# Optimization experiments

Hardware: AMD Instinct MI355X
Metric: run time of the kernel (lower is better)

## Reference

```python
import jax, jax.numpy as jnp
import numpy as np

NUM_ITERS = 3
NUM_SLOTS = 8
D = 128
MLP_HIDDEN = 128
EPS = 1e-8
LN_EPS = 1e-5
B, N = 64, 4096


def _layer_norm(x, g, b):
    m = jnp.mean(x, axis=-1, keepdims=True)
    v = jnp.mean(jnp.square(x - m), axis=-1, keepdims=True)
    return (x - m) * jax.lax.rsqrt(v + LN_EPS) * g + b


def setup_inputs() -> dict:
    key = jax.random.key(0)
    ks = jax.random.split(key, 16)
    s = 1.0 / np.sqrt(D)
    inp = {
        "x": jax.random.normal(ks[0], (B, N, D), jnp.float32),
        "slots_init": jax.random.normal(ks[1], (B, NUM_SLOTS, D), jnp.float32),
        "Wq": jax.random.normal(ks[2], (D, D), jnp.float32) * s,
        "bq": jnp.zeros((D,), jnp.float32),
        "Wk": jax.random.normal(ks[3], (D, D), jnp.float32) * s,
        "bk": jnp.zeros((D,), jnp.float32),
        "Wv": jax.random.normal(ks[4], (D, D), jnp.float32) * s,
        "bv": jnp.zeros((D,), jnp.float32),
        "g_in": jnp.ones((D,), jnp.float32), "b_in": jnp.zeros((D,), jnp.float32),
        "g_slot": jnp.ones((D,), jnp.float32), "b_slot": jnp.zeros((D,), jnp.float32),
        "g_mlp": jnp.ones((D,), jnp.float32), "b_mlp": jnp.zeros((D,), jnp.float32),
        "W1": jax.random.normal(ks[5], (MLP_HIDDEN, D), jnp.float32) * s,
        "b1": jnp.zeros((MLP_HIDDEN,), jnp.float32),
        "W2": jax.random.normal(ks[6], (D, MLP_HIDDEN), jnp.float32) * (1.0 / np.sqrt(MLP_HIDDEN)),
        "b2": jnp.zeros((D,), jnp.float32),
        "W_ih": jax.random.normal(ks[7], (3 * D, D), jnp.float32) * s,
        "W_hh": jax.random.normal(ks[8], (3 * D, D), jnp.float32) * s,
        "b_ih": jnp.zeros((3 * D,), jnp.float32),
        "b_hh": jnp.zeros((3 * D,), jnp.float32),
    }
    return inp


def _gru_cell(x, h, W_ih, W_hh, b_ih, b_hh):
    # torch.nn.GRUCell semantics
    gi = x @ W_ih.T + b_ih          # [.., 3D]
    gh = h @ W_hh.T + b_hh
    i_r, i_z, i_n = jnp.split(gi, 3, axis=-1)
    h_r, h_z, h_n = jnp.split(gh, 3, axis=-1)
    r = jax.nn.sigmoid(i_r + h_r)
    z = jax.nn.sigmoid(i_z + h_z)
    n = jnp.tanh(i_n + r * h_n)
    return (1.0 - z) * n + z * h


def reference(x, slots_init, Wq, bq, Wk, bk, Wv, bv, g_in, b_in, g_slot, b_slot,
              g_mlp, b_mlp, W1, b1, W2, b2, W_ih, W_hh, b_ih, b_hh):
    xn = _layer_norm(x, g_in, b_in)                 # [B,N,D]
    keys = xn @ Wk.T + bk                            # [B,N,D]
    values = xn @ Wv.T + bv                          # [B,N,D]
    scale = D ** -0.5
    slots = slots_init                               # [B,K,D]
    for _ in range(NUM_ITERS):
        prev = slots
        s = _layer_norm(slots, g_slot, b_slot)
        q = s @ Wq.T + bq                            # [B,K,D]
        logits = jnp.einsum('bid,bkd->bik', q, keys) * scale  # [B,K,N]
        attn = jax.nn.softmax(logits, axis=1)        # softmax over SLOT axis
        attn = attn + EPS
        attn = attn / jnp.sum(attn, axis=-1, keepdims=True)
        updates = jnp.einsum('bkd,bik->bid', values, attn)     # [B,K,D]
        slots = _gru_cell(updates.reshape(-1, D), prev.reshape(-1, D),
                          W_ih, W_hh, b_ih, b_hh).reshape(x.shape[0], -1, D)
        h = jax.nn.relu(_layer_norm(slots, g_mlp, b_mlp) @ W1.T + b1)
        slots = slots + (h @ W2.T + b2)
    return slots
```

## Files before the change

### kernel.cpp

```cpp
#include <hip/hip_runtime.h>
#include <hip/hip_bf16.h>

#define B_ 64
#define N_ 4096
#define KS 8
#define NCH 16
#define TP 136
#define LNEPS 1e-5f
#define EPSA 1e-8f
#define SCALE 0.08838834764831845f

typedef short short8  __attribute__((ext_vector_type(8)));
typedef short short4v __attribute__((ext_vector_type(4)));
typedef float f32x4   __attribute__((ext_vector_type(4)));

__device__ __forceinline__ unsigned short f2bf(float f) {
  union { float f; unsigned u; } v; v.f = f;
  unsigned r = v.u + 0x7fffu + ((v.u >> 16) & 1u);
  return (unsigned short)(r >> 16);
}
__device__ __forceinline__ float bflo(unsigned u) {
  union { unsigned u; float f; } c; c.u = u << 16; return c.f;
}
__device__ __forceinline__ float bfhi(unsigned u) {
  union { unsigned u; float f; } c; c.u = u & 0xffff0000u; return c.f;
}
__device__ __forceinline__ float sigmf(float x) { return 1.f / (1.f + __expf(-x)); }

__global__ __launch_bounds__(256) void prep_big(
    const float* __restrict__ Wih, const float* __restrict__ Whh,
    const float* __restrict__ Wq,  const float* __restrict__ Wk,
    const float* __restrict__ Wv,  const float* __restrict__ W1,
    const float* __restrict__ W2,
    const float* __restrict__ g_slot, const float* __restrict__ g_mlp,
    float* __restrict__ WgT, float* __restrict__ Mq,
    float* __restrict__ W1gT, float* __restrict__ W2T)
{
  int id = blockIdx.x * 256 + threadIdx.x;
  if (id < 49152) {
    int j = id >> 7, d = id & 127;
    float a = 0.f;
    for (int k = 0; k < 128; k++) a += Wih[j*128 + k] * Wv[k*128 + d];
    WgT[d*768 + j] = a;
  } else if (id < 65536) {
    int k = id - 49152; int d = k >> 7, t = k & 127;
    float a = 0.f;
    for (int j = 0; j < 128; j++) a += Wk[j*128 + t] * Wq[j*128 + d];
    Mq[d*128 + t] = a * SCALE * g_slot[d];
  } else if (id < 114688) {
    int k = id - 65536; int j = k >> 7, d = k & 127;
    WgT[d*768 + 384 + j] = Whh[j*128 + d];
  } else if (id < 131072) {
    int k = id - 114688; int t = k >> 7, d = k & 127;
    W1gT[d*128 + t] = W1[t*128 + d] * g_mlp[d];
  } else if (id < 147456) {
    int k = id - 131072; int t = k >> 7, d = k & 127;
    W2T[d*128 + t] = W2[t*128 + d];
  }
}

__global__ __launch_bounds__(256) void prep_small(
    const float* __restrict__ Wq, const float* __restrict__ Wk,
    const float* __restrict__ Wih, const float* __restrict__ W1,
    const float* __restrict__ bq, const float* __restrict__ bk,
    const float* __restrict__ bv, const float* __restrict__ b_ih,
    const float* __restrict__ b_hh, const float* __restrict__ b1,
    const float* __restrict__ b_mlp, const float* __restrict__ b_slot,
    const float* __restrict__ g_slot,
    float* __restrict__ cq_vec, float* __restrict__ wqcg,
    float* __restrict__ qc0g, float* __restrict__ bg, float* __restrict__ b1f)
{
  __shared__ float u[128], wqcr[128];
  int t = threadIdx.x;
  if (t < 128) {
    float a = bq[t];
    for (int d = 0; d < 128; d++) a += Wq[t*128 + d] * b_slot[d];
    u[t] = a;
  } else {
    int d = t - 128;
    float a = 0.f;
    for (int j = 0; j < 128; j++) a += Wq[j*128 + d] * bk[j];
    wqcr[d] = a * SCALE;
  }
  __syncthreads();
  if (t < 128) {
    float a = 0.f;
    for (int j = 0; j < 128; j++) a += Wk[j*128 + t] * u[j];
    cq_vec[t] = a * SCALE;
    wqcg[t] = wqcr[t] * g_slot[t];
  } else {
    int d = t - 128;
    float a = b1[d];
    for (int k = 0; k < 128; k++) a += W1[d*128 + k] * b_mlp[k];
    b1f[d] = a;
  }
  if (t < 64) {
    float v = wqcr[t]*b_slot[t] + wqcr[t+64]*b_slot[t+64]
            + SCALE*(bq[t]*bk[t] + bq[t+64]*bk[t+64]);
    #pragma unroll
    for (int st = 1; st < 64; st <<= 1) v += __shfl_xor(v, st);
    if (t == 0) *qc0g = v;
  }
  #pragma unroll
  for (int p = 0; p < 3; p++) {
    int j = t + p*256;
    if (j < 384) {
      float a = b_ih[j];
      for (int k = 0; k < 128; k++) a += Wih[j*128 + k] * bv[k];
      bg[j] = a;
    } else if (j < 768) {
      bg[j] = b_hh[j - 384];
    }
  }
}

__global__ __launch_bounds__(256) void ln_kernel(
    const float* __restrict__ x, const float* __restrict__ g_in, const float* __restrict__ b_in,
    unsigned short* __restrict__ xn)
{
  int tid = threadIdx.x;
  int rw = tid >> 2, cp = tid & 3;
  size_t row = (size_t)blockIdx.x * 64 + rw;
  const float* xrow = x + row * 128;
  float4 v[8];
  float s = 0.f, s2 = 0.f;
  #pragma unroll
  for (int i = 0; i < 8; i++) {
    v[i] = *(const float4*)(xrow + (cp + 4*i)*4);
    s  += v[i].x + v[i].y + v[i].z + v[i].w;
    s2 += v[i].x*v[i].x + v[i].y*v[i].y + v[i].z*v[i].z + v[i].w*v[i].w;
  }
  s += __shfl_xor(s, 1); s2 += __shfl_xor(s2, 1);
  s += __shfl_xor(s, 2); s2 += __shfl_xor(s2, 2);
  float mean = s * (1.f/128.f);
  float rstd = rsqrtf(s2 * (1.f/128.f) - mean*mean + LNEPS);
  #pragma unroll
  for (int i = 0; i < 8; i++) {
    int col = (cp + 4*i)*4;
    float4 gg = *(const float4*)(g_in + col);
    float4 bb = *(const float4*)(b_in + col);
    short4v pk;
    pk[0] = (short)f2bf((v[i].x - mean)*rstd*gg.x + bb.x);
    pk[1] = (short)f2bf((v[i].y - mean)*rstd*gg.y + bb.y);
    pk[2] = (short)f2bf((v[i].z - mean)*rstd*gg.z + bb.z);
    pk[3] = (short)f2bf((v[i].w - mean)*rstd*gg.w + bb.w);
    *(short4v*)(xn + row*128 + col) = pk;
  }
}

__global__ __launch_bounds__(64) void q_init_kernel(
    const float* __restrict__ slots_in, const float* __restrict__ Mq,
    const float* __restrict__ cq_vec, const float* __restrict__ wqcg,
    const float* __restrict__ qc0g,
    float* __restrict__ qt, float* __restrict__ qc)
{
  __shared__ float lnr[128];
  int row = blockIdx.x, t = threadIdx.x;
  float a = slots_in[row*128 + t], b = slots_in[row*128 + 64 + t];
  float s = a + b, s2 = a*a + b*b;
  #pragma unroll
  for (int st = 1; st < 64; st <<= 1) { s += __shfl_xor(s, st); s2 += __shfl_xor(s2, st); }
  float mean = s * (1.f/128.f);
  float rstd = rsqrtf(s2 * (1.f/128.f) - mean*mean + LNEPS);
  lnr[t] = (a - mean)*rstd; lnr[t+64] = (b - mean)*rstd;
  __syncthreads();
  float a0 = cq_vec[t], a1 = cq_vec[t+64];
  for (int d = 0; d < 128; d++) {
    float l = lnr[d];
    a0 += Mq[d*128 + t] * l;
    a1 += Mq[d*128 + 64 + t] * l;
  }
  qt[row*128 + t] = a0; qt[row*128 + 64 + t] = a1;
  float vq = wqcg[t]*lnr[t] + wqcg[t+64]*lnr[t+64];
  #pragma unroll
  for (int st = 1; st < 64; st <<= 1) vq += __shfl_xor(vq, st);
  if (t == 0) qc[row] = vq + *qc0g;
}

__global__ __launch_bounds__(256) void attn_kernel(
    const unsigned short* __restrict__ xn,
    const float* __restrict__ qt, const float* __restrict__ qc,
    float* __restrict__ Upart, float* __restrict__ Spart)
{
  __shared__ union ShMem {
    unsigned short xt[4][16][TP];
    float ured[4][8][128];
  } sh;
  __shared__ __align__(16) float pb[4][16][8];
  __shared__ float sred[4][8];

  const int tid = threadIdx.x;
  const int w = tid >> 6, lane = tid & 63;
  const int chunk = blockIdx.x, batch = blockIdx.y;
  const int m = lane & 15, quad = lane >> 4;

  short8 afrag[4];
  if (m < KS) {
    const float* qp = qt + (batch*KS + m)*128 + quad*8;
    #pragma unroll
    for (int kc = 0; kc < 4; kc++) {
      short8 a;
      #pragma unroll
      for (int j = 0; j < 8; j++) a[j] = (short)f2bf(qp[kc*32 + j]);
      afrag[kc] = a;
    }
  } else {
    #pragma unroll
    for (int kc = 0; kc < 4; kc++) {
      short8 a;
      #pragma unroll
      for (int j = 0; j < 8; j++) a[j] = 0;
      afrag[kc] = a;
    }
  }
  float creg[4];
  #pragma unroll
  for (int r = 0; r < 4; r++) creg[r] = qc[batch*KS + ((quad*4 + r) & 7)];

  float u0[8], u1[8], sac[4];
  #pragma unroll
  for (int i = 0; i < 8; i++) { u0[i] = 0.f; u1[i] = 0.f; }
  #pragma unroll
  for (int r = 0; r < 4; r++) sac[r] = 0.f;

  const unsigned short* xbase =
      xn + ((size_t)batch*N_ + chunk*256 + w*64 + m)*128 + quad*8;

  short8 cur[4], nxt[4];
  #pragma unroll
  for (int kc = 0; kc < 4; kc++) cur[kc] = *(const short8*)(xbase + kc*32);

  for (int g = 0; g < 4; g++) {
    if (g < 3) {
      #pragma unroll
      for (int kc = 0; kc < 4; kc++)
        nxt[kc] = *(const short8*)(xbase + (g+1)*2048 + kc*32);
    }
    #pragma unroll
    for (int kc = 0; kc < 4; kc++)
      *(short8*)&sh.xt[w][m][kc*32 + quad*8] = cur[kc];

    f32x4 acc = {0.f, 0.f, 0.f, 0.f};
    #pragma unroll
    for (int kc = 0; kc < 4; kc++)
      acc = __builtin_amdgcn_mfma_f32_16x16x32_bf16(afrag[kc], cur[kc], acc, 0, 0, 0);

    float l[4], o[4];
    #pragma unroll
    for (int r = 0; r < 4; r++) l[r] = acc[r] + creg[r];
    #pragma unroll
    for (int r = 0; r < 4; r++) o[r] = __shfl_xor(l[r], 16);
    float mx = fmaxf(fmaxf(fmaxf(l[0], l[1]), fmaxf(l[2], l[3])),
                     fmaxf(fmaxf(o[0], o[1]), fmaxf(o[2], o[3])));
    float e0 = __expf(l[0]-mx), e1 = __expf(l[1]-mx), e2 = __expf(l[2]-mx), e3 = __expf(l[3]-mx);
    float den = e0+e1+e2+e3 + __expf(o[0]-mx)+__expf(o[1]-mx)+__expf(o[2]-mx)+__expf(o[3]-mx);
    float rd = 1.f / den;
    float p0 = e0*rd + EPSA, p1 = e1*rd + EPSA, p2 = e2*rd + EPSA, p3 = e3*rd + EPSA;
    sac[0] += p0; sac[1] += p1; sac[2] += p2; sac[3] += p3;
    if (lane < 32) {
      float4 pv; pv.x = p0; pv.y = p1; pv.z = p2; pv.w = p3;
      *(float4*)&pb[w][m][quad*4] = pv;
    }

    #pragma unroll
    for (int t = 0; t < 16; t++) {
      float4 pA = *(const float4*)&pb[w][t][0];
      float4 pB = *(const float4*)&pb[w][t][4];
      unsigned vp = *(const unsigned*)&sh.xt[w][t][lane*2];
      float f0 = bflo(vp), f1 = bfhi(vp);
      u0[0] += pA.x*f0; u1[0] += pA.x*f1;
      u0[1] += pA.y*f0; u1[1] += pA.y*f1;
      u0[2] += pA.z*f0; u1[2] += pA.z*f1;
      u0[3] += pA.w*f0; u1[3] += pA.w*f1;
      u0[4] += pB.x*f0; u1[4] += pB.x*f1;
      u0[5] += pB.y*f0; u1[5] += pB.y*f1;
      u0[6] += pB.z*f0; u1[6] += pB.z*f1;
      u0[7] += pB.w*f0; u1[7] += pB.w*f1;
    }
    #pragma unroll
    for (int kc = 0; kc < 4; kc++) cur[kc] = nxt[kc];
  }

  #pragma unroll
  for (int st = 1; st < 16; st <<= 1) {
    #pragma unroll
    for (int r = 0; r < 4; r++) sac[r] += __shfl_xor(sac[r], st);
  }
  if (lane == 0)  { sred[w][0]=sac[0]; sred[w][1]=sac[1]; sred[w][2]=sac[2]; sred[w][3]=sac[3]; }
  if (lane == 16) { sred[w][4]=sac[0]; sred[w][5]=sac[1]; sred[w][6]=sac[2]; sred[w][7]=sac[3]; }

  __syncthreads();
  #pragma unroll
  for (int i = 0; i < 8; i++)
    *(float2*)&sh.ured[w][i][lane*2] = make_float2(u0[i], u1[i]);
  __syncthreads();

  {
    const float* ur = &sh.ured[0][0][0];
    int i4 = tid * 4;
    float4 a = *(const float4*)(ur + i4);
    float4 b = *(const float4*)(ur + 1024 + i4);
    float4 c = *(const float4*)(ur + 2048 + i4);
    float4 d = *(const float4*)(ur + 3072 + i4);
    float4 o4;
    o4.x = a.x+b.x+c.x+d.x; o4.y = a.y+b.y+c.y+d.y;
    o4.z = a.z+b.z+c.z+d.z; o4.w = a.w+b.w+c.w+d.w;
    *(float4*)(Upart + (size_t)(batch*NCH + chunk)*1024 + i4) = o4;
    if (tid < 8)
      Spart[(batch*NCH + chunk)*8 + tid] =
        sred[0][tid] + sred[1][tid] + sred[2][tid] + sred[3][tid];
  }
}

__global__ __launch_bounds__(256) void update_kernel(
    const float* __restrict__ slots_in, float* __restrict__ slots_out,
    const float* __restrict__ Upart, const float* __restrict__ Spart,
    const float* __restrict__ WgT, const float* __restrict__ bg,
    const float* __restrict__ W1gT, const float* __restrict__ b1f,
    const float* __restrict__ W2T, const float* __restrict__ b2,
    const float* __restrict__ Mq, const float* __restrict__ cq_vec,
    const float* __restrict__ wqcg, const float* __restrict__ qc0g,
    float* __restrict__ qt, float* __restrict__ qc)
{
  __shared__ float bu[128], hb[128], gg[768];
  __shared__ float s1[128], lnr[128], hmv[128], s2v[128], lnr2[128];
  __shared__ float stats[2], sSum;
  int row = blockIdx.x, t = threadIdx.x;
  int batch = row >> 3, slot = row & 7;

  float usum = 0.f;
  if (t < 128) {
    const float* Up = Upart + ((size_t)(batch*NCH)*8 + slot)*128 + t;
    #pragma unroll
    for (int c = 0; c < NCH; c++) usum += Up[(size_t)c*1024];
  } else {
    hb[t-128] = slots_in[row*128 + (t-128)];
    if (t < 192) {
      int l2 = t - 128;
      float sv = (l2 < NCH) ? Spart[(batch*NCH + l2)*8 + slot] : 0.f;
      #pragma unroll
      for (int st = 1; st < 16; st <<= 1) sv += __shfl_xor(sv, st);
      if (l2 == 0) sSum = sv;
    }
  }
  __syncthreads();
  if (t < 128) bu[t] = usum / sSum;
  __syncthreads();
  {
    float a0 = bg[t], a1 = bg[t+256], a2 = bg[t+512];
    const float* v1p = (t < 128) ? bu : hb;
    for (int d = 0; d < 128; d++) {
      float sd = bu[d], hd = hb[d], vd = v1p[d];
      const float* wr = WgT + d*768 + t;
      a0 += sd * wr[0];
      a1 += vd * wr[256];
      a2 += hd * wr[512];
    }
    gg[t] = a0; gg[t+256] = a1; gg[t+512] = a2;
  }
  __syncthreads();
  if (t < 128) {
    float r = sigmf(gg[t] + gg[384+t]);
    float z = sigmf(gg[128+t] + gg[512+t]);
    float n = tanhf(gg[256+t] + r * gg[640+t]);
    s1[t] = (1.f - z)*n + z*hb[t];
  }
  __syncthreads();
  if (t < 64) {
    float a = s1[t], b = s1[t+64];
    float s = a + b, s2 = a*a + b*b;
    #pragma unroll
    for (int st = 1; st < 64; st <<= 1) { s += __shfl_xor(s, st); s2 += __shfl_xor(s2, st); }
    if (t == 0) { float mean = s*(1.f/128.f); stats[0] = mean;
                  stats[1] = rsqrtf(s2*(1.f/128.f) - mean*mean + LNEPS); }
  }
  __syncthreads();
  if (t < 128) lnr[t] = (s1[t] - stats[0])*stats[1];
  __syncthreads();
  if (t < 128) {
    float a = b1f[t];
    for (int d = 0; d < 128; d++) a += W1gT[d*128 + t]*lnr[d];
    hmv[t] = fmaxf(a, 0.f);
  }
  __syncthreads();
  if (t < 128) {
    float a = s1[t] + b2[t];
    for (int d = 0; d < 128; d++) a += W2T[d*128 + t]*hmv[d];
    s2v[t] = a;
    slots_out[row*128 + t] = a;
  }
  __syncthreads();
  if (t < 64) {
    float a = s2v[t], b = s2v[t+64];
    float s = a + b, s2 = a*a + b*b;
    #pragma unroll
    for (int st = 1; st < 64; st <<= 1) { s += __shfl_xor(s, st); s2 += __shfl_xor(s2, st); }
    if (t == 0) { float mean = s*(1.f/128.f); stats[0] = mean;
                  stats[1] = rsqrtf(s2*(1.f/128.f) - mean*mean + LNEPS); }
  }
  __syncthreads();
  if (t < 128) lnr2[t] = (s2v[t] - stats[0])*stats[1];
  __syncthreads();
  if (t < 128) {
    float a = cq_vec[t];
    for (int d = 0; d < 128; d++) a += Mq[d*128 + t]*lnr2[d];
    qt[row*128 + t] = a;
  }
  if (t < 64) {
    float v = wqcg[t]*lnr2[t] + wqcg[t+64]*lnr2[t+64];
    #pragma unroll
    for (int st = 1; st < 64; st <<= 1) v += __shfl_xor(v, st);
    if (t == 0) qc[row] = v + *qc0g;
  }
}

extern "C" void kernel_launch(void* const* d_in, const int* in_sizes, int n_in,
                              void* d_out, int out_size, void* d_ws, size_t ws_size,
                              hipStream_t stream) {
  const float* x          = (const float*)d_in[0];
  const float* slots_init = (const float*)d_in[1];
  const float* Wq   = (const float*)d_in[2];
  const float* bq   = (const float*)d_in[3];
  const float* Wk   = (const float*)d_in[4];
  const float* bk   = (const float*)d_in[5];
  const float* Wv   = (const float*)d_in[6];
  const float* bv   = (const float*)d_in[7];
  const float* g_in = (const float*)d_in[8];
  const float* b_in = (const float*)d_in[9];
  const float* g_slot = (const float*)d_in[10];
  const float* b_slot = (const float*)d_in[11];
  const float* g_mlp  = (const float*)d_in[12];
  const float* b_mlp  = (const float*)d_in[13];
  const float* W1   = (const float*)d_in[14];
  const float* b1   = (const float*)d_in[15];
  const float* W2   = (const float*)d_in[16];
  const float* b2   = (const float*)d_in[17];
  const float* Wih  = (const float*)d_in[18];
  const float* Whh  = (const float*)d_in[19];
  const float* b_ih = (const float*)d_in[20];
  const float* b_hh = (const float*)d_in[21];

  char* p = (char*)d_ws;
  unsigned short* xn = (unsigned short*)p; p += (size_t)B_*N_*128*2;
  float* qt    = (float*)p; p += (size_t)B_*KS*128*4;
  float* qc    = (float*)p; p += (size_t)B_*KS*4 + 1024;
  float* slots = (float*)p; p += (size_t)B_*KS*128*4;
  float* Upart = (float*)p; p += (size_t)B_*NCH*KS*128*4;
  float* Spart = (float*)p; p += (size_t)B_*NCH*KS*4 + 1024;
  float* WgT   = (float*)p; p += 98304*4;
  float* Mq    = (float*)p; p += 16384*4;
  float* W1gT  = (float*)p; p += 16384*4;
  float* W2T   = (float*)p; p += 16384*4;
  float* cq_vec= (float*)p; p += 128*4;
  float* wqcg  = (float*)p; p += 128*4;
  float* qc0g  = (float*)p; p += 256;
  float* bg    = (float*)p; p += 768*4;
  float* b1f   = (float*)p; p += 128*4;

  ln_kernel<<<4096, 256, 0, stream>>>(x, g_in, b_in, xn);
  prep_big<<<576, 256, 0, stream>>>(Wih, Whh, Wq, Wk, Wv, W1, W2, g_slot, g_mlp,
                                    WgT, Mq, W1gT, W2T);
  prep_small<<<1, 256, 0, stream>>>(Wq, Wk, Wih, W1, bq, bk, bv, b_ih, b_hh, b1,
                                    b_mlp, b_slot, g_slot, cq_vec, wqcg, qc0g, bg, b1f);
  q_init_kernel<<<512, 64, 0, stream>>>(slots_init, Mq, cq_vec, wqcg, qc0g, qt, qc);

  attn_kernel<<<dim3(NCH, B_), 256, 0, stream>>>(xn, qt, qc, Upart, Spart);
  update_kernel<<<512, 256, 0, stream>>>(slots_init, slots, Upart, Spart,
      WgT, bg, W1gT, b1f, W2T, b2, Mq, cq_vec, wqcg, qc0g, qt, qc);

  attn_kernel<<<dim3(NCH, B_), 256, 0, stream>>>(xn, qt, qc, Upart, Spart);
  update_kernel<<<512, 256, 0, stream>>>(slots, slots, Upart, Spart,
      WgT, bg, W1gT, b1f, W2T, b2, Mq, cq_vec, wqcg, qc0g, qt, qc);

  attn_kernel<<<dim3(NCH, B_), 256, 0, stream>>>(xn, qt, qc, Upart, Spart);
  update_kernel<<<512, 256, 0, stream>>>(slots, (float*)d_out, Upart, Spart,
      WgT, bg, W1gT, b1f, W2T, b2, Mq, cq_vec, wqcg, qc0g, qt, qc);

  (void)in_sizes; (void)n_in; (void)out_size; (void)ws_size;
}
```

Before: 395.1 us.

## Fuse input layernorm into first attention pass and halve attention chunk count

Input layernorm now runs inside the first attention kernel: it reads fp32 x, normalizes each row into shared memory as bf16, writes xn back for later iterations, and consumes it directly. This removes the separate LN kernel and the first re-read of xn. Attention chunks drop from 16 to 8 per batch, so each block handles 512 tokens with double-buffered prefetch two groups ahead. The two prep kernels are merged into one launch. The trade-off is fewer blocks (512), which lowers parallelism, and the fused first pass carries heavier per-block work.

Result: slower. 1.240 ms (+213.8%).

```diff
diff --git a/kernel.cpp b/kernel.cpp
--- a/kernel.cpp
+++ b/kernel.cpp
@@ -4,7 +4,7 @@
 #define B_ 64
 #define N_ 4096
 #define KS 8
-#define NCH 16
+#define ACH 8
 #define TP 136
 #define LNEPS 1e-5f
 #define EPSA 1e-8f
@@ -27,15 +27,66 @@
 }
 __device__ __forceinline__ float sigmf(float x) { return 1.f / (1.f + __expf(-x)); }
 
-__global__ __launch_bounds__(256) void prep_big(
+__global__ __launch_bounds__(256) void prep_kernel(
     const float* __restrict__ Wih, const float* __restrict__ Whh,
     const float* __restrict__ Wq,  const float* __restrict__ Wk,
     const float* __restrict__ Wv,  const float* __restrict__ W1,
     const float* __restrict__ W2,
     const float* __restrict__ g_slot, const float* __restrict__ g_mlp,
+    const float* __restrict__ bq, const float* __restrict__ bk,
+    const float* __restrict__ bv, const float* __restrict__ b_ih,
+    const float* __restrict__ b_hh, const float* __restrict__ b1,
+    const float* __restrict__ b_mlp, const float* __restrict__ b_slot,
     float* __restrict__ WgT, float* __restrict__ Mq,
-    float* __restrict__ W1gT, float* __restrict__ W2T)
-{
+    float* __restrict__ W1gT, float* __restrict__ W2T,
+    float* __restrict__ cq_vec, float* __restrict__ wqcg,
+    float* __restrict__ qc0g, float* __restrict__ bg, float* __restrict__ b1f)
+{
+  if (blockIdx.x == 576) {
+    __shared__ float u[128], wqcr[128];
+    int t = threadIdx.x;
+    if (t < 128) {
+      float a = bq[t];
+      for (int d = 0; d < 128; d++) a += Wq[t*128 + d] * b_slot[d];
+      u[t] = a;
+    } else {
+      int d = t - 128;
+      float a = 0.f;
+      for (int j = 0; j < 128; j++) a += Wq[j*128 + d] * bk[j];
+      wqcr[d] = a * SCALE;
+    }
+    __syncthreads();
+    if (t < 128) {
+      float a = 0.f;
+      for (int j = 0; j < 128; j++) a += Wk[j*128 + t] * u[j];
+      cq_vec[t] = a * SCALE;
+      wqcg[t] = wqcr[t] * g_slot[t];
+    } else {
+      int d = t - 128;
+      float a = b1[d];
+      for (int k = 0; k < 128; k++) a += W1[d*128 + k] * b_mlp[k];
+      b1f[d] = a;
+    }
+    if (t < 64) {
+      float v = wqcr[t]*b_slot[t] + wqcr[t+64]*b_slot[t+64]
+              + SCALE*(bq[t]*bk[t] + bq[t+64]*bk[t+64]);
+      #pragma unroll
+      for (int st = 1; st < 64; st <<= 1) v += __shfl_xor(v, st);
+      if (t == 0) *qc0g = v;
+    }
+    #pragma unroll
+    for (int p = 0; p < 3; p++) {
+      int j = t + p*256;
+      if (j < 384) {
+        float a = b_ih[j];
+        for (int k = 0; k < 128; k++) a += Wih[j*128 + k] * bv[k];
+        bg[j] = a;
+      } else if (j < 768) {
+        bg[j] = b_hh[j - 384];
+      }
+    }
+    return;
+  }
   int id = blockIdx.x * 256 + threadIdx.x;
   if (id < 49152) {
     int j = id >> 7, d = id & 127;
@@ -59,95 +110,6 @@
   }
 }
 
-__global__ __launch_bounds__(256) void prep_small(
-    const float* __restrict__ Wq, const float* __restrict__ Wk,
-    const float* __restrict__ Wih, const float* __restrict__ W1,
-    const float* __restrict__ bq, const float* __restrict__ bk,
-    const float* __restrict__ bv, const float* __restrict__ b_ih,
-    const float* __restrict__ b_hh, const float* __restrict__ b1,
-    const float* __restrict__ b_mlp, const float* __restrict__ b_slot,
-    const float* __restrict__ g_slot,
-    float* __restrict__ cq_vec, float* __restrict__ wqcg,
-    float* __restrict__ qc0g, float* __restrict__ bg, float* __restrict__ b1f)
-{
-  __shared__ float u[128], wqcr[128];
-  int t = threadIdx.x;
-  if (t < 128) {
-    float a = bq[t];
-    for (int d = 0; d < 128; d++) a += Wq[t*128 + d] * b_slot[d];
-    u[t] = a;
-  } else {
-    int d = t - 128;
-    float a = 0.f;
-    for (int j = 0; j < 128; j++) a += Wq[j*128 + d] * bk[j];
-    wqcr[d] = a * SCALE;
-  }
-  __syncthreads();
-  if (t < 128) {
-    float a = 0.f;
-    for (int j = 0; j < 128; j++) a += Wk[j*128 + t] * u[j];
-    cq_vec[t] = a * SCALE;
-    wqcg[t] = wqcr[t] * g_slot[t];
-  } else {
-    int d = t - 128;
-    float a = b1[d];
-    for (int k = 0; k < 128; k++) a += W1[d*128 + k] * b_mlp[k];
-    b1f[d] = a;
-  }
-  if (t < 64) {
-    float v = wqcr[t]*b_slot[t] + wqcr[t+64]*b_slot[t+64]
-            + SCALE*(bq[t]*bk[t] + bq[t+64]*bk[t+64]);
-    #pragma unroll
-    for (int st = 1; st < 64; st <<= 1) v += __shfl_xor(v, st);
-    if (t == 0) *qc0g = v;
-  }
-  #pragma unroll
-  for (int p = 0; p < 3; p++) {
-    int j = t + p*256;
-    if (j < 384) {
-      float a = b_ih[j];
-      for (int k = 0; k < 128; k++) a += Wih[j*128 + k] * bv[k];
-      bg[j] = a;
-    } else if (j < 768) {
-      bg[j] = b_hh[j - 384];
-    }
-  }
-}
-
-__global__ __launch_bounds__(256) void ln_kernel(
-    const float* __restrict__ x, const float* __restrict__ g_in, const float* __restrict__ b_in,
-    unsigned short* __restrict__ xn)
-{
-  int tid = threadIdx.x;
-  int rw = tid >> 2, cp = tid & 3;
-  size_t row = (size_t)blockIdx.x * 64 + rw;
-  const float* xrow = x + row * 128;
-  float4 v[8];
-  float s = 0.f, s2 = 0.f;
-  #pragma unroll
-  for (int i = 0; i < 8; i++) {
-    v[i] = *(const float4*)(xrow + (cp + 4*i)*4);
-    s  += v[i].x + v[i].y + v[i].z + v[i].w;
-    s2 += v[i].x*v[i].x + v[i].y*v[i].y + v[i].z*v[i].z + v[i].w*v[i].w;
-  }
-  s += __shfl_xor(s, 1); s2 += __shfl_xor(s2, 1);
-  s += __shfl_xor(s, 2); s2 += __shfl_xor(s2, 2);
-  float mean = s * (1.f/128.f);
-  float rstd = rsqrtf(s2 * (1.f/128.f) - mean*mean + LNEPS);
-  #pragma unroll
-  for (int i = 0; i < 8; i++) {
-    int col = (cp + 4*i)*4;
-    float4 gg = *(const float4*)(g_in + col);
-    float4 bb = *(const float4*)(b_in + col);
-    short4v pk;
-    pk[0] = (short)f2bf((v[i].x - mean)*rstd*gg.x + bb.x);
-    pk[1] = (short)f2bf((v[i].y - mean)*rstd*gg.y + bb.y);
-    pk[2] = (short)f2bf((v[i].z - mean)*rstd*gg.z + bb.z);
-    pk[3] = (short)f2bf((v[i].w - mean)*rstd*gg.w + bb.w);
-    *(short4v*)(xn + row*128 + col) = pk;
-  }
-}
-
 __global__ __launch_bounds__(64) void q_init_kernel(
     const float* __restrict__ slots_in, const float* __restrict__ Mq,
     const float* __restrict__ cq_vec, const float* __restrict__ wqcg,
@@ -177,24 +139,87 @@
   if (t == 0) qc[row] = vq + *qc0g;
 }
 
-__global__ __launch_bounds__(256) void attn_kernel(
-    const unsigned short* __restrict__ xn,
+__device__ __forceinline__ void attn_group_core(
+    unsigned short (*xtw)[TP], float (*pbw)[8],
+    const short8* afrag, const float* creg, const short8* bfrag,
+    int lane, int m, int quad,
+    float* sac, float* u0, float* u1)
+{
+  f32x4 acc = {0.f, 0.f, 0.f, 0.f};
+  #pragma unroll
+  for (int kc = 0; kc < 4; kc++)
+    acc = __builtin_amdgcn_mfma_f32_16x16x32_bf16(afrag[kc], bfrag[kc], acc, 0, 0, 0);
+  float l[4], o[4];
+  #pragma unroll
+  for (int r = 0; r < 4; r++) l[r] = acc[r] + creg[r];
+  #pragma unroll
+  for (int r = 0; r < 4; r++) o[r] = __shfl_xor(l[r], 16);
+  float mx = fmaxf(fmaxf(fmaxf(l[0], l[1]), fmaxf(l[2], l[3])),
+                   fmaxf(fmaxf(o[0], o[1]), fmaxf(o[2], o[3])));
+  float e0 = __expf(l[0]-mx), e1 = __expf(l[1]-mx), e2 = __expf(l[2]-mx), e3 = __expf(l[3]-mx);
+  float den = e0+e1+e2+e3 + __expf(o[0]-mx)+__expf(o[1]-mx)+__expf(o[2]-mx)+__expf(o[3]-mx);
+  float rd = 1.f / den;
+  float p0 = e0*rd + EPSA, p1 = e1*rd + EPSA, p2 = e2*rd + EPSA, p3 = e3*rd + EPSA;
+  sac[0] += p0; sac[1] += p1; sac[2] += p2; sac[3] += p3;
+  if (lane < 32) {
+    float4 pv; pv.x = p0; pv.y = p1; pv.z = p2; pv.w = p3;
+    *(float4*)&pbw[m][quad*4] = pv;
+  }
+  #pragma unroll
+  for (int t = 0; t < 16; t++) {
+    float4 pA = *(const float4*)&pbw[t][0];
+    float4 pB = *(const float4*)&pbw[t][4];
+    unsigned vp = *(const unsigned*)&xtw[t][lane*2];
+    float f0 = bflo(vp), f1 = bfhi(vp);
+    u0[0] += pA.x*f0; u1[0] += pA.x*f1;
+    u0[1] += pA.y*f0; u1[1] += pA.y*f1;
+    u0[2] += pA.z*f0; u1[2] += pA.z*f1;
+    u0[3] += pA.w*f0; u1[3] += pA.w*f1;
+    u0[4] += pB.x*f0; u1[4] += pB.x*f1;
+    u0[5] += pB.y*f0; u1[5] += pB.y*f1;
+    u0[6] += pB.z*f0; u1[6] += pB.z*f1;
+    u0[7] += pB.w*f0; u1[7] += pB.w*f1;
+  }
+}
+
+__device__ __forceinline__ void attn_epilogue(
+    float* uredf, float (*sred)[8], float* sac, float* u0, float* u1,
+    int tid, int w, int lane, int chunk, int batch,
+    float* __restrict__ Upart, float* __restrict__ Spart)
+{
+  #pragma unroll
+  for (int st = 1; st < 16; st <<= 1) {
+    #pragma unroll
+    for (int r = 0; r < 4; r++) sac[r] += __shfl_xor(sac[r], st);
+  }
+  if (lane == 0)  { sred[w][0]=sac[0]; sred[w][1]=sac[1]; sred[w][2]=sac[2]; sred[w][3]=sac[3]; }
+  if (lane == 16) { sred[w][4]=sac[0]; sred[w][5]=sac[1]; sred[w][6]=sac[2]; sred[w][7]=sac[3]; }
+  __syncthreads();
+  float* uw = uredf + w*1024;
+  #pragma unroll
+  for (int i = 0; i < 8; i++)
+    *(float2*)&uw[i*128 + lane*2] = make_float2(u0[i], u1[i]);
+  __syncthreads();
+  {
+    int i4 = tid * 4;
+    float4 a = *(const float4*)(uredf + i4);
+    float4 b = *(const float4*)(uredf + 1024 + i4);
+    float4 c = *(const float4*)(uredf + 2048 + i4);
+    float4 d = *(const float4*)(uredf + 3072 + i4);
+    float4 o4;
+    o4.x = a.x+b.x+c.x+d.x; o4.y = a.y+b.y+c.y+d.y;
+    o4.z = a.z+b.z+c.z+d.z; o4.w = a.w+b.w+c.w+d.w;
+    *(float4*)(Upart + (size_t)(batch*ACH + chunk)*1024 + i4) = o4;
+    if (tid < 8)
+      Spart[(batch*ACH + chunk)*8 + tid] =
+        sred[0][tid] + sred[1][tid] + sred[2][tid] + sred[3][tid];
+  }
+}
+
+__device__ __forceinline__ void load_afrag(
     const float* __restrict__ qt, const float* __restrict__ qc,
-    float* __restrict__ Upart, float* __restrict__ Spart)
-{
-  __shared__ union ShMem {
-    unsigned short xt[4][16][TP];
-    float ured[4][8][128];
-  } sh;
-  __shared__ __align__(16) float pb[4][16][8];
-  __shared__ float sred[4][8];
-
-  const int tid = threadIdx.x;
-  const int w = tid >> 6, lane = tid & 63;
-  const int chunk = blockIdx.x, batch = blockIdx.y;
-  const int m = lane & 15, quad = lane >> 4;
-
-  short8 afrag[4];
+    int batch, int m, int quad, short8* afrag, float* creg)
+{
   if (m < KS) {
     const float* qp = qt + (batch*KS + m)*128 + quad*8;
     #pragma unroll
@@ -213,9 +238,29 @@
       afrag[kc] = a;
     }
   }
-  float creg[4];
   #pragma unroll
   for (int r = 0; r < 4; r++) creg[r] = qc[batch*KS + ((quad*4 + r) & 7)];
+}
+
+__global__ __launch_bounds__(256) void attn_kernel(
+    const unsigned short* __restrict__ xn,
+    const float* __restrict__ qt, const float* __restrict__ qc,
+    float* __restrict__ Upart, float* __restrict__ Spart)
+{
+  __shared__ union ShMem {
+    unsigned short xt[4][16][TP];
+    float ured[4096];
+  } sh;
+  __shared__ __align__(16) float pb[4][16][8];
+  __shared__ float sred[4][8];
+
+  const int tid = threadIdx.x;
+  const int w = tid >> 6, lane = tid & 63;
+  const int chunk = blockIdx.x, batch = blockIdx.y;
+  const int m = lane & 15, quad = lane >> 4;
+
+  short8 afrag[4]; float creg[4];
+  load_afrag(qt, qc, batch, m, quad, afrag, creg);
 
   float u0[8], u1[8], sac[4];
   #pragma unroll
@@ -223,93 +268,112 @@
   #pragma unroll
   for (int r = 0; r < 4; r++) sac[r] = 0.f;
 
-  const unsigned short* xbase =
-      xn + ((size_t)batch*N_ + chunk*256 + w*64 + m)*128 + quad*8;
-
-  short8 cur[4], nxt[4];
-  #pragma unroll
-  for (int kc = 0; kc < 4; kc++) cur[kc] = *(const short8*)(xbase + kc*32);
-
-  for (int g = 0; g < 4; g++) {
-    if (g < 3) {
+  const unsigned short* xb =
+      xn + ((size_t)batch*N_ + chunk*512 + w*128 + m)*128 + quad*8;
+
+  short8 buf[2][4];
+  #pragma unroll
+  for (int kc = 0; kc < 4; kc++) buf[0][kc] = *(const short8*)(xb + kc*32);
+  #pragma unroll
+  for (int kc = 0; kc < 4; kc++) buf[1][kc] = *(const short8*)(xb + 2048 + kc*32);
+
+  for (int g = 0; g < 8; g++) {
+    const int b = g & 1;
+    short8 cur[4];
+    #pragma unroll
+    for (int kc = 0; kc < 4; kc++) cur[kc] = buf[b][kc];
+    if (g < 6) {
       #pragma unroll
       for (int kc = 0; kc < 4; kc++)
-        nxt[kc] = *(const short8*)(xbase + (g+1)*2048 + kc*32);
+        buf[b][kc] = *(const short8*)(xb + (g+2)*2048 + kc*32);
     }
     #pragma unroll
     for (int kc = 0; kc < 4; kc++)
       *(short8*)&sh.xt[w][m][kc*32 + quad*8] = cur[kc];
-
-    f32x4 acc = {0.f, 0.f, 0.f, 0.f};
+    attn_group_core(sh.xt[w], pb[w], afrag, creg, cur, lane, m, quad, sac, u0, u1);
+  }
+  attn_epilogue(sh.ured, sred, sac, u0, u1, tid, w, lane, chunk, batch, Upart, Spart);
+}
+
+__global__ __launch_bounds__(256) void attn0_kernel(
+    const float* __restrict__ x, const float* __restrict__ g_in, const float* __restrict__ b_in,
+    unsigned short* __restrict__ xn,
+    const float* __restrict__ qt, const float* __restrict__ qc,
+    float* __restrict__ Upart, float* __restrict__ Spart)
+{
+  __shared__ union ShMem {
+    unsigned short xt[4][16][TP];
+    float ured[4096];
+  } sh;
+  __shared__ __align__(16) float pb[4][16][8];
+  __shared__ float sred[4][8];
+
+  const int tid = threadIdx.x;
+  const int w = tid >> 6, lane = tid & 63;
+  const int chunk = blockIdx.x, batch = blockIdx.y;
+  const int m = lane & 15, quad = lane >> 4;
+
+  short8 afrag[4]; float creg[4];
+  load_afrag(qt, qc, batch, m, quad, afrag, creg);
+
+  float u0[8], u1[8], sac[4];
+  #pragma unroll
+  for (int i = 0; i < 8; i++) { u0[i] = 0.f; u1[i] = 0.f; }
+  #pragma unroll
+  for (int r = 0; r < 4; r++) sac[r] = 0.f;
+
+  const int rw = lane >> 2, cp = lane & 3;
+  const float* xr0 = x + ((size_t)batch*N_ + chunk*512 + w*128 + rw) * 128;
+
+  float4 buf[2][8];
+  #pragma unroll
+  for (int i = 0; i < 8; i++) buf[0][i] = *(const float4*)(xr0 + (cp + 4*i)*4);
+
+  for (int g = 0; g < 8; g++) {
+    const int b = g & 1;
+    if (g < 7) {
+      #pragma unroll
+      for (int i = 0; i < 8; i++)
+        buf[b^1][i] = *(const float4*)(xr0 + (g+1)*2048 + (cp + 4*i)*4);
+    }
+    float s = 0.f, s2 = 0.f;
+    #pragma unroll
+    for (int i = 0; i < 8; i++) {
+      float4 v = buf[b][i];
+      s  += v.x + v.y + v.z + v.w;
+      s2 += v.x*v.x + v.y*v.y + v.z*v.z + v.w*v.w;
+    }
+    s += __shfl_xor(s, 1); s2 += __shfl_xor(s2, 1);
+    s += __shfl_xor(s, 2); s2 += __shfl_xor(s2, 2);
+    float mean = s * (1.f/128.f);
+    float rstd = rsqrtf(s2 * (1.f/128.f) - mean*mean + LNEPS);
+    #pragma unroll
+    for (int i = 0; i < 8; i++) {
+      int col = (cp + 4*i)*4;
+      float4 v  = buf[b][i];
+      float4 gg = *(const float4*)(g_in + col);
+      float4 bb = *(const float4*)(b_in + col);
+      short4v pk;
+      pk[0] = (short)f2bf((v.x - mean)*rstd*gg.x + bb.x);
+      pk[1] = (short)f2bf((v.y - mean)*rstd*gg.y + bb.y);
+      pk[2] = (short)f2bf((v.z - mean)*rstd*gg.z + bb.z);
+      pk[3] = (short)f2bf((v.w - mean)*rstd*gg.w + bb.w);
+      *(short4v*)&sh.xt[w][rw][col] = pk;
+    }
+    const int tb = chunk*512 + w*128 + g*16;
+    #pragma unroll
+    for (int p = 0; p < 4; p++) {
+      int idx = p*64 + lane; int rr = idx >> 4, c16 = idx & 15;
+      int4 dv = *(const int4*)&sh.xt[w][rr][c16*8];
+      *(int4*)(xn + ((size_t)batch*N_ + tb + rr)*128 + c16*8) = dv;
+    }
+    short8 bfrag[4];
     #pragma unroll
     for (int kc = 0; kc < 4; kc++)
-      acc = __builtin_amdgcn_mfma_f32_16x16x32_bf16(afrag[kc], cur[kc], acc, 0, 0, 0);
-
-    float l[4], o[4];
-    #pragma unroll
-    for (int r = 0; r < 4; r++) l[r] = acc[r] + creg[r];
-    #pragma unroll
-    for (int r = 0; r < 4; r++) o[r] = __shfl_xor(l[r], 16);
-    float mx = fmaxf(fmaxf(fmaxf(l[0], l[1]), fmaxf(l[2], l[3])),
-                     fmaxf(fmaxf(o[0], o[1]), fmaxf(o[2], o[3])));
-    float e0 = __expf(l[0]-mx), e1 = __expf(l[1]-mx), e2 = __expf(l[2]-mx), e3 = __expf(l[3]-mx);
-    float den = e0+e1+e2+e3 + __expf(o[0]-mx)+__expf(o[1]-mx)+__expf(o[2]-mx)+__expf(o[3]-mx);
-    float rd = 1.f / den;
-    float p0 = e0*rd + EPSA, p1 = e1*rd + EPSA, p2 = e2*rd + EPSA, p3 = e3*rd + EPSA;
-    sac[0] += p0; sac[1] += p1; sac[2] += p2; sac[3] += p3;
-    if (lane < 32) {
-      float4 pv; pv.x = p0; pv.y = p1; pv.z = p2; pv.w = p3;
-      *(float4*)&pb[w][m][quad*4] = pv;
-    }
-
-    #pragma unroll
-    for (int t = 0; t < 16; t++) {
-      float4 pA = *(const float4*)&pb[w][t][0];
-      float4 pB = *(const float4*)&pb[w][t][4];
-      unsigned vp = *(const unsigned*)&sh.xt[w][t][lane*2];
-      float f0 = bflo(vp), f1 = bfhi(vp);
-      u0[0] += pA.x*f0; u1[0] += pA.x*f1;
-      u0[1] += pA.y*f0; u1[1] += pA.y*f1;
-      u0[2] += pA.z*f0; u1[2] += pA.z*f1;
-      u0[3] += pA.w*f0; u1[3] += pA.w*f1;
-      u0[4] += pB.x*f0; u1[4] += pB.x*f1;
-      u0[5] += pB.y*f0; u1[5] += pB.y*f1;
-      u0[6] += pB.z*f0; u1[6] += pB.z*f1;
-      u0[7] += pB.w*f0; u1[7] += pB.w*f1;
-    }
-    #pragma unroll
-    for (int kc = 0; kc < 4; kc++) cur[kc] = nxt[kc];
-  }
-
-  #pragma unroll
-  for (int st = 1; st < 16; st <<= 1) {
-    #pragma unroll
-    for (int r = 0; r < 4; r++) sac[r] += __shfl_xor(sac[r], st);
-  }
-  if (lane == 0)  { sred[w][0]=sac[0]; sred[w][1]=sac[1]; sred[w][2]=sac[2]; sred[w][3]=sac[3]; }
-  if (lane == 16) { sred[w][4]=sac[0]; sred[w][5]=sac[1]; sred[w][6]=sac[2]; sred[w][7]=sac[3]; }
-
-  __syncthreads();
-  #pragma unroll
-  for (int i = 0; i < 8; i++)
-    *(float2*)&sh.ured[w][i][lane*2] = make_float2(u0[i], u1[i]);
-  __syncthreads();
-
-  {
-    const float* ur = &sh.ured[0][0][0];
-    int i4 = tid * 4;
-    float4 a = *(const float4*)(ur + i4);
-    float4 b = *(const float4*)(ur + 1024 + i4);
-    float4 c = *(const float4*)(ur + 2048 + i4);
-    float4 d = *(const float4*)(ur + 3072 + i4);
-    float4 o4;
-    o4.x = a.x+b.x+c.x+d.x; o4.y = a.y+b.y+c.y+d.y;
-    o4.z = a.z+b.z+c.z+d.z; o4.w = a.w+b.w+c.w+d.w;
-    *(float4*)(Upart + (size_t)(batch*NCH + chunk)*1024 + i4) = o4;
-    if (tid < 8)
-      Spart[(batch*NCH + chunk)*8 + tid] =
-        sred[0][tid] + sred[1][tid] + sred[2][tid] + sred[3][tid];
-  }
+      bfrag[kc] = *(const short8*)&sh.xt[w][m][kc*32 + quad*8];
+    attn_group_core(sh.xt[w], pb[w], afrag, creg, bfrag, lane, m, quad, sac, u0, u1);
+  }
+  attn_epilogue(sh.ured, sred, sac, u0, u1, tid, w, lane, chunk, batch, Upart, Spart);
 }
 
 __global__ __launch_bounds__(256) void update_kernel(
@@ -330,16 +394,16 @@
 
   float usum = 0.f;
   if (t < 128) {
-    const float* Up = Upart + ((size_t)(batch*NCH)*8 + slot)*128 + t;
-    #pragma unroll
-    for (int c = 0; c < NCH; c++) usum += Up[(size_t)c*1024];
+    const float* Up = Upart + ((size_t)(batch*ACH)*8 + slot)*128 + t;
+    #pragma unroll
+    for (int c = 0; c < ACH; c++) usum += Up[(size_t)c*1024];
   } else {
     hb[t-128] = slots_in[row*128 + (t-128)];
     if (t < 192) {
       int l2 = t - 128;
-      float sv = (l2 < NCH) ? Spart[(batch*NCH + l2)*8 + slot] : 0.f;
+      float sv = (l2 < ACH) ? Spart[(batch*ACH + l2)*8 + slot] : 0.f;
       #pragma unroll
-      for (int st = 1; st < 16; st <<= 1) sv += __shfl_xor(sv, st);
+      for (int st = 1; st < 8; st <<= 1) sv += __shfl_xor(sv, st);
       if (l2 == 0) sSum = sv;
     }
   }
@@ -445,8 +509,8 @@
   float* qt    = (float*)p; p += (size_t)B_*KS*128*4;
   float* qc    = (float*)p; p += (size_t)B_*KS*4 + 1024;
   float* slots = (float*)p; p += (size_t)B_*KS*128*4;
-  float* Upart = (float*)p; p += (size_t)B_*NCH*KS*128*4;
-  float* Spart = (float*)p; p += (size_t)B_*NCH*KS*4 + 1024;
+  float* Upart = (float*)p; p += (size_t)B_*ACH*KS*128*4;
+  float* Spart = (float*)p; p += (size_t)B_*ACH*KS*4 + 1024;
   float* WgT   = (float*)p; p += 98304*4;
   float* Mq    = (float*)p; p += 16384*4;
   float* W1gT  = (float*)p; p += 16384*4;
@@ -457,22 +521,20 @@
   float* bg    = (float*)p; p += 768*4;
   float* b1f   = (float*)p; p += 128*4;
 
-  ln_kernel<<<4096, 256, 0, stream>>>(x, g_in, b_in, xn);
-  prep_big<<<576, 256, 0, stream>>>(Wih, Whh, Wq, Wk, Wv, W1, W2, g_slot, g_mlp,
-                                    WgT, Mq, W1gT, W2T);
-  prep_small<<<1, 256, 0, stream>>>(Wq, Wk, Wih, W1, bq, bk, bv, b_ih, b_hh, b1,
-                                    b_mlp, b_slot, g_slot, cq_vec, wqcg, qc0g, bg, b1f);
+  prep_kernel<<<577, 256, 0, stream>>>(Wih, Whh, Wq, Wk, Wv, W1, W2, g_slot, g_mlp,
+                                       bq, bk, bv, b_ih, b_hh, b1, b_mlp, b_slot,
+                                       WgT, Mq, W1gT, W2T, cq_vec, wqcg, qc0g, bg, b1f);
   q_init_kernel<<<512, 64, 0, stream>>>(slots_init, Mq, cq_vec, wqcg, qc0g, qt, qc);
 
-  attn_kernel<<<dim3(NCH, B_), 256, 0, stream>>>(xn, qt, qc, Upart, Spart);
+  attn0_kernel<<<dim3(ACH, B_), 256, 0, stream>>>(x, g_in, b_in, xn, qt, qc, Upart, Spart);
   update_kernel<<<512, 256, 0, stream>>>(slots_init, slots, Upart, Spart,
       WgT, bg, W1gT, b1f, W2T, b2, Mq, cq_vec, wqcg, qc0g, qt, qc);
 
-  attn_kernel<<<dim3(NCH, B_), 256, 0, stream>>>(xn, qt, qc, Upart, Spart);
+  attn_kernel<<<dim3(ACH, B_), 256, 0, stream>>>(xn, qt, qc, Upart, Spart);
   update_kernel<<<512, 256, 0, stream>>>(slots, slots, Upart, Spart,
       WgT, bg, W1gT, b1f, W2T, b2, Mq, cq_vec, wqcg, qc0g, qt, qc);
 
-  attn_kernel<<<dim3(NCH, B_), 256, 0, stream>>>(xn, qt, qc, Upart, Spart);
+  attn_kernel<<<dim3(ACH, B_), 256, 0, stream>>>(xn, qt, qc, Upart, Spart);
   update_kernel<<<512, 256, 0, stream>>>(slots, (float*)d_out, Upart, Spart,
       WgT, bg, W1gT, b1f, W2T, b2, Mq, cq_vec, wqcg, qc0g, qt, qc);
 
```
